# Kernel optimization log

Measured on AMD Instinct MI355X. Metric: run time of the kernel, lower is better.

## Reference

```python
import jax, jax.numpy as jnp
import numpy as np

F_IN = 512
F_OUT = 512
HEADS = 8  # all heads share the same weights in the original module
NEG_SLOPE = 0.01  # nn.LeakyReLU default
MASK_VAL = -1.0e10


def setup_inputs() -> dict:
    key = jax.random.key(0)
    ks = jax.random.split(key, 6)
    B, N = 8, 2048
    X_input = jax.random.normal(ks[0], (B, N, F_IN), dtype=jnp.float32)
    u = jax.random.uniform(ks[1], (B, N, N), dtype=jnp.float32)
    A_input = jnp.maximum((u < 0.02).astype(jnp.float32), jnp.eye(N, dtype=jnp.float32)[None])
    # learned params (nn.Linear stores W as [out,in]; we use [in,out] with x @ W)
    Wk = jax.random.normal(ks[2], (F_IN, F_OUT), dtype=jnp.float32) / np.sqrt(F_IN).astype(np.float32)
    bk = jnp.zeros((F_OUT,), dtype=jnp.float32)
    ws = jax.random.normal(ks[3], (F_OUT,), dtype=jnp.float32) / np.sqrt(F_OUT).astype(np.float32)
    bs = jnp.zeros((), dtype=jnp.float32)
    wn = jax.random.normal(ks[4], (F_OUT,), dtype=jnp.float32) / np.sqrt(F_OUT).astype(np.float32)
    bn = jnp.zeros((), dtype=jnp.float32)
    return {"X_input": X_input, "A_input": A_input, "Wk": Wk, "bk": bk,
            "ws": ws, "bs": bs, "wn": wn, "bn": bn}


def reference(X_input, A_input, Wk, bk, ws, bs, wn, bn):
    # shared projection (identical across all heads in the original loop)
    feat = jnp.einsum('bnf,fg->bng', X_input, Wk) + bk          # [B,N,F_]
    a_self = jnp.einsum('bng,g->bn', feat, ws) + bs             # [B,N]
    a_neigh = jnp.einsum('bng,g->bn', feat, wn) + bn            # [B,N]
    # torch.bmm([B,N,1],[B,1,N]) -> multiplicative outer product score
    att = jax.nn.leaky_relu(a_self[:, :, None] * a_neigh[:, None, :], NEG_SLOPE)
    att = att + MASK_VAL * (1.0 - A_input)                      # [B,N,N]
    p = jax.nn.softmax(att, axis=-1)
    nf = jnp.einsum('bij,bjg->big', p, feat)                    # [B,N,F_]
    # concat of HEADS identical head outputs, then tanh
    out = jnp.tanh(jnp.concatenate([nf] * HEADS, axis=-1))      # [B,N,HEADS*F_]
    return out
```

## Files before the change

### kernel.cpp

```cpp
#include <hip/hip_runtime.h>

#define NEG_SLOPE 0.01f
#define B_ 8
#define N_ 2048
#define F_ 512
#define M_ (B_ * N_)

typedef unsigned short u16;
typedef __attribute__((ext_vector_type(8))) unsigned short u16x8;
typedef __attribute__((ext_vector_type(8))) __bf16 bf16x8;
typedef __attribute__((ext_vector_type(4))) float f32x4;

__device__ __forceinline__ u16 f2bf(float f) {
    unsigned u = __float_as_uint(f);
    u += 0x7FFFu + ((u >> 16) & 1u);
    return (u16)(u >> 16);
}
__device__ __forceinline__ float bf2f(u16 h) {
    return __uint_as_float(((unsigned)h) << 16);
}

__device__ __forceinline__ f32x4 mfma16(u16x8 a, u16x8 b, f32x4 c) {
    return __builtin_amdgcn_mfma_f32_16x16x32_bf16(
        __builtin_bit_cast(bf16x8, a), __builtin_bit_cast(bf16x8, b), c, 0, 0, 0);
}

__device__ __forceinline__ void load_lds16(const void* g, void* l) {
    __builtin_amdgcn_global_load_lds(
        (__attribute__((address_space(1))) void*)(void*)g,
        (__attribute__((address_space(3))) void*)l, 16, 0, 0);
}

__global__ __launch_bounds__(256) void convert_wkt(const float* __restrict__ Wk,
                                                   u16* __restrict__ Whi,
                                                   u16* __restrict__ Wlo) {
    const int id = blockIdx.x * 256 + threadIdx.x;
    const int k = id & 511;
    const int n = id >> 9;
    const float f = Wk[k * 512 + n];
    const u16 h = f2bf(f);
    Whi[id] = h;
    Wlo[id] = f2bf(f - bf2f(h));
}

__global__ __launch_bounds__(256) void prep(const float* __restrict__ Wk,
                                            const float* __restrict__ bk,
                                            const float* __restrict__ ws,
                                            const float* __restrict__ bs,
                                            const float* __restrict__ wn,
                                            const float* __restrict__ bn,
                                            float* __restrict__ ws2,
                                            float* __restrict__ wn2,
                                            float* __restrict__ csn) {
    const int t = threadIdx.x, lane = t & 63, w = t >> 6;
    const int bid = blockIdx.x;
    if (bid >= 256) {
        if (w == 0) {
            const int sel = bid - 256;
            const float* vec = sel ? wn : ws;
            const float4 b0 = *(const float4*)(bk + lane * 8);
            const float4 b1 = *(const float4*)(bk + lane * 8 + 4);
            const float4 v0 = *(const float4*)(vec + lane * 8);
            const float4 v1 = *(const float4*)(vec + lane * 8 + 4);
            float d = b0.x * v0.x + b0.y * v0.y + b0.z * v0.z + b0.w * v0.w +
                      b1.x * v1.x + b1.y * v1.y + b1.z * v1.z + b1.w * v1.w;
#pragma unroll
            for (int m = 32; m; m >>= 1) d += __shfl_xor(d, m);
            if (lane == 0) csn[sel] = d + (sel ? bn[0] : bs[0]);
        }
        return;
    }
    const int W = bid * 4 + w;
    const int k = W & 511;
    const float* vec = (W < 512) ? ws : wn;
    const float4 w0 = *(const float4*)(Wk + (size_t)k * 512 + lane * 8);
    const float4 w1 = *(const float4*)(Wk + (size_t)k * 512 + lane * 8 + 4);
    const float4 v0 = *(const float4*)(vec + lane * 8);
    const float4 v1 = *(const float4*)(vec + lane * 8 + 4);
    float d = w0.x * v0.x + w0.y * v0.y + w0.z * v0.z + w0.w * v0.w +
              w1.x * v1.x + w1.y * v1.y + w1.z * v1.z + w1.w * v1.w;
#pragma unroll
    for (int m = 32; m; m >>= 1) d += __shfl_xor(d, m);
    if (lane == 0) ((W < 512) ? ws2 : wn2)[k] = d;
}

__global__ __launch_bounds__(256) void dots_x(const float* __restrict__ X,
                                              const float* __restrict__ ws2,
                                              const float* __restrict__ wn2,
                                              const float* __restrict__ csn,
                                              float* __restrict__ a_self,
                                              float* __restrict__ a_neigh) {
    const int t = threadIdx.x, lane = t & 63, w = t >> 6;
    const int row = blockIdx.x * 4 + w;
    const float4 f0 = *(const float4*)(X + (size_t)row * 512 + lane * 8);
    const float4 f1 = *(const float4*)(X + (size_t)row * 512 + lane * 8 + 4);
    const float fv[8] = {f0.x, f0.y, f0.z, f0.w, f1.x, f1.y, f1.z, f1.w};
    const float4 sa = *(const float4*)(ws2 + lane * 8);
    const float4 sb = *(const float4*)(ws2 + lane * 8 + 4);
    const float4 na = *(const float4*)(wn2 + lane * 8);
    const float4 nb = *(const float4*)(wn2 + lane * 8 + 4);
    float ds = fv[0] * sa.x + fv[1] * sa.y + fv[2] * sa.z + fv[3] * sa.w +
               fv[4] * sb.x + fv[5] * sb.y + fv[6] * sb.z + fv[7] * sb.w;
    float dn = fv[0] * na.x + fv[1] * na.y + fv[2] * na.z + fv[3] * na.w +
               fv[4] * nb.x + fv[5] * nb.y + fv[6] * nb.z + fv[7] * nb.w;
#pragma unroll
    for (int m = 32; m; m >>= 1) {
        ds += __shfl_xor(ds, m);
        dn += __shfl_xor(dn, m);
    }
    if (lane == 0) {
        a_self[row] = ds + csn[0];
        a_neigh[row] = dn + csn[1];
    }
}

__global__ __launch_bounds__(256) void gemm_feat(const float* __restrict__ X,
                                                 const u16* __restrict__ Whi,
                                                 const u16* __restrict__ Wlo,
                                                 const float* __restrict__ bk,
                                                 u16* __restrict__ feat) {
    __shared__ u16 Ah[128 * 64];
    __shared__ u16 Al[128 * 64];
    __shared__ u16 Bh[128 * 64];
    __shared__ u16 Bl[128 * 64];
    const int t = threadIdx.x;
    const int lane = t & 63;
    const int w = t >> 6;
    const int bid = blockIdx.x;
    const int tm = (bid & 7) * 16 + (bid >> 5);
    const int tn = (bid >> 3) & 3;
    const int wr = w >> 1, wc = w & 1;

    f32x4 acc[4][4];
#pragma unroll
    for (int m = 0; m < 4; ++m)
#pragma unroll
        for (int n = 0; n < 4; ++n) acc[m][n] = {0.f, 0.f, 0.f, 0.f};

    const int lrow = lane >> 3;
    const int lcol = (lane & 7) * 8;
    const u16* BhBase = Whi + ((size_t)(tn * 128 + w * 8 + lrow)) * 512 + lcol;
    const u16* BlBase = Wlo + ((size_t)(tn * 128 + w * 8 + lrow)) * 512 + lcol;
    u16* BhW = Bh + (w * 8) * 64;
    u16* BlW = Bl + (w * 8) * 64;

    const int arow = t >> 3;
    const int akk = (t & 7) * 8;
    const float* Abase = X + ((size_t)(tm * 128 + arow)) * 512 + akk;
    u16* AhW = Ah + arow * 64 + akk;
    u16* AlW = Al + arow * 64 + akk;

    for (int k0 = 0; k0 < 512; k0 += 64) {
#pragma unroll
        for (int iss = 0; iss < 4; ++iss) {
            load_lds16(BhBase + (size_t)(iss * 32) * 512 + k0, BhW + iss * 32 * 64);
            load_lds16(BlBase + (size_t)(iss * 32) * 512 + k0, BlW + iss * 32 * 64);
        }
#pragma unroll
        for (int p = 0; p < 4; ++p) {
            const float4 x0 = *(const float4*)(Abase + (size_t)(p * 32) * 512 + k0);
            const float4 x1 = *(const float4*)(Abase + (size_t)(p * 32) * 512 + k0 + 4);
            const float xv[8] = {x0.x, x0.y, x0.z, x0.w, x1.x, x1.y, x1.z, x1.w};
            u16x8 hi, lo;
#pragma unroll
            for (int e = 0; e < 8; ++e) {
                const u16 h = f2bf(xv[e]);
                hi[e] = h;
                lo[e] = f2bf(xv[e] - bf2f(h));
            }
            *(u16x8*)(AhW + p * 32 * 64) = hi;
            *(u16x8*)(AlW + p * 32 * 64) = lo;
        }
        __syncthreads();
#pragma unroll
        for (int kk = 0; kk < 64; kk += 32) {
            u16x8 ah[4], al[4], bh[4], bl[4];
            const int aoff = kk + (lane >> 4) * 8;
#pragma unroll
            for (int m = 0; m < 4; ++m) {
                const int r = (wr * 64 + m * 16 + (lane & 15)) * 64 + aoff;
                ah[m] = *(const u16x8*)(Ah + r);
                al[m] = *(const u16x8*)(Al + r);
            }
#pragma unroll
            for (int n = 0; n < 4; ++n) {
                const int r = (wc * 64 + n * 16 + (lane & 15)) * 64 + aoff;
                bh[n] = *(const u16x8*)(Bh + r);
                bl[n] = *(const u16x8*)(Bl + r);
            }
#pragma unroll
            for (int m = 0; m < 4; ++m)
#pragma unroll
                for (int n = 0; n < 4; ++n) {
                    acc[m][n] = mfma16(ah[m], bh[n], acc[m][n]);
                    acc[m][n] = mfma16(ah[m], bl[n], acc[m][n]);
                    acc[m][n] = mfma16(al[m], bh[n], acc[m][n]);
                }
        }
        __syncthreads();
    }

    const int crow0 = tm * 128 + wr * 64;
    const int ccol0 = tn * 128 + wc * 64;
#pragma unroll
    for (int n = 0; n < 4; ++n) {
        const int gc = ccol0 + n * 16 + (lane & 15);
        const float bkv = bk[gc];
#pragma unroll
        for (int m = 0; m < 4; ++m) {
            const int gr = crow0 + m * 16 + (lane >> 4) * 4;
#pragma unroll
            for (int r = 0; r < 4; ++r)
                feat[(size_t)(gr + r) * 512 + gc] = f2bf(acc[m][n][r] + bkv);
        }
    }
}

__global__ __launch_bounds__(256) void attn_row(const float* __restrict__ A,
                                                const u16* __restrict__ feat,
                                                const float* __restrict__ a_self,
                                                const float* __restrict__ a_neigh,
                                                float* __restrict__ out) {
    const int bid = blockIdx.x;
    const int row = (bid & 7) * N_ + (bid >> 3);
    const int b = bid & 7;
    const int t = threadIdx.x;
    const int lane = t & 63, w = t >> 6;

    __shared__ int   lj[N_];
    __shared__ float lsv[N_];
    __shared__ int   wtot[4];
    __shared__ float wred[8];
    __shared__ float nfw[4][F_];

    const float asi = a_self[row];

    const float4* Arow = (const float4*)(A + (size_t)row * N_);
    const float4* An   = (const float4*)(a_neigh + b * N_);
    const float4 a0 = Arow[t * 2], a1 = Arow[t * 2 + 1];
    const float4 n0 = An[t * 2],   n1 = An[t * 2 + 1];
    const float av[8] = {a0.x, a0.y, a0.z, a0.w, a1.x, a1.y, a1.z, a1.w};
    const float nv[8] = {n0.x, n0.y, n0.z, n0.w, n1.x, n1.y, n1.z, n1.w};
    float sv[8];
    int cnt = 0;
    float mloc = -3.0e38f;
#pragma unroll
    for (int e = 0; e < 8; ++e) {
        float s = asi * nv[e];
        s = s > 0.f ? s : NEG_SLOPE * s;
        sv[e] = s;
        if (av[e] != 0.f) { ++cnt; mloc = fmaxf(mloc, s); }
    }
    int v = cnt;
#pragma unroll
    for (int off = 1; off < 64; off <<= 1) {
        const int u = __shfl_up(v, off);
        if (lane >= off) v += u;
    }
#pragma unroll
    for (int m = 32; m; m >>= 1) mloc = fmaxf(mloc, __shfl_xor(mloc, m));
    if (lane == 63) wtot[w] = v;
    if (lane == 0) wred[w] = mloc;
    __syncthreads();
    int base = v - cnt;
#pragma unroll
    for (int i = 0; i < 4; ++i) base += (i < w) ? wtot[i] : 0;
    const int total = wtot[0] + wtot[1] + wtot[2] + wtot[3];
    const float mx = fmaxf(fmaxf(wred[0], wred[1]), fmaxf(wred[2], wred[3]));
    int pos = base;
#pragma unroll
    for (int e = 0; e < 8; ++e) {
        if (av[e] != 0.f) { lj[pos] = t * 8 + e; lsv[pos] = sv[e]; ++pos; }
    }
    __syncthreads();

    float ssum = 0.f;
    for (int k = t; k < total; k += 256) {
        const float wv = __expf(lsv[k] - mx);
        lsv[k] = wv;
        ssum += wv;
    }
#pragma unroll
    for (int m = 32; m; m >>= 1) ssum += __shfl_xor(ssum, m);
    if (lane == 0) wred[4 + w] = ssum;
    __syncthreads();
    const float inv = 1.f / (wred[4] + wred[5] + wred[6] + wred[7]);

    const u16* frow = feat + (size_t)b * N_ * F_ + lane * 8;
    float acc[8] = {0.f, 0.f, 0.f, 0.f, 0.f, 0.f, 0.f, 0.f};
    int k = w;
    for (; k + 4 < total; k += 8) {
        const size_t j0 = (size_t)lj[k] * F_, j1 = (size_t)lj[k + 4] * F_;
        const float p0 = lsv[k], p1 = lsv[k + 4];
        const u16x8 v0 = *(const u16x8*)(frow + j0);
        const u16x8 v1 = *(const u16x8*)(frow + j1);
#pragma unroll
        for (int e = 0; e < 8; ++e) acc[e] += p0 * bf2f(v0[e]) + p1 * bf2f(v1[e]);
    }
    if (k < total) {
        const size_t j0 = (size_t)lj[k] * F_;
        const float p0 = lsv[k];
        const u16x8 v0 = *(const u16x8*)(frow + j0);
#pragma unroll
        for (int e = 0; e < 8; ++e) acc[e] += p0 * bf2f(v0[e]);
    }
#pragma unroll
    for (int e = 0; e < 8; ++e) nfw[w][lane * 8 + e] = acc[e];
    __syncthreads();

    const int f0 = t * 2;
    const float nf0 = (nfw[0][f0] + nfw[1][f0]) + (nfw[2][f0] + nfw[3][f0]);
    const float nf1 = (nfw[0][f0 + 1] + nfw[1][f0 + 1]) + (nfw[2][f0 + 1] + nfw[3][f0 + 1]);
    const float o0 = tanhf(nf0 * inv);
    const float o1 = tanhf(nf1 * inv);
    const float2 o = make_float2(o0, o1);
    float* obase = out + (size_t)row * (8 * F_) + f0;
#pragma unroll
    for (int h = 0; h < 8; ++h) *(float2*)(obase + h * F_) = o;
}

extern "C" void kernel_launch(void* const* d_in, const int* in_sizes, int n_in,
                              void* d_out, int out_size, void* d_ws, size_t ws_size,
                              hipStream_t stream) {
    const float* X  = (const float*)d_in[0];
    const float* A  = (const float*)d_in[1];
    const float* Wk = (const float*)d_in[2];
    const float* bk = (const float*)d_in[3];
    const float* ws = (const float*)d_in[4];
    const float* bs = (const float*)d_in[5];
    const float* wn = (const float*)d_in[6];
    const float* bn = (const float*)d_in[7];
    float* out = (float*)d_out;

    char* wsb = (char*)d_ws;
    u16*   feat    = (u16*)(wsb);
    u16*   Whi     = (u16*)(wsb + 16777216);
    u16*   Wlo     = (u16*)(wsb + 17301504);
    float* a_self  = (float*)(wsb + 17825792);
    float* a_neigh = (float*)(wsb + 17891328);
    float* ws2     = (float*)(wsb + 17956864);
    float* wn2     = (float*)(wsb + 17958912);
    float* csn     = (float*)(wsb + 17960960);

    convert_wkt<<<dim3(1024),  dim3(256), 0, stream>>>(Wk, Whi, Wlo);
    prep       <<<dim3(258),   dim3(256), 0, stream>>>(Wk, bk, ws, bs, wn, bn, ws2, wn2, csn);
    dots_x     <<<dim3(4096),  dim3(256), 0, stream>>>(X, ws2, wn2, csn, a_self, a_neigh);
    gemm_feat  <<<dim3(512),   dim3(256), 0, stream>>>(X, Whi, Wlo, bk, feat);
    attn_row   <<<dim3(16384), dim3(256), 0, stream>>>(A, feat, a_self, a_neigh, out);
}
```

Before: 161.9 us.

## Switch feature GEMM to single-pass fp16 MFMA with swizzled LDS, fuse prep kernels

Replaces the three-pass bf16 hi/lo split GEMM with a single fp16 MFMA pass, which cuts both the MFMA count and the LDS traffic. It swizzles the LDS layout to avoid bank conflicts and merges the weight conversion and prep kernels into a single launch. Feat is now stored as fp16. The attention kernel now computes the exponentials during compaction and stores neighbor indices as u16, which removes a barrier and a pass over LDS. The GEMM loses precision compared with the split-bf16 scheme, and fp16 carries a risk of range overflow.

```diff
diff --git a/kernel.cpp b/kernel.cpp
--- a/kernel.cpp
+++ b/kernel.cpp
@@ -4,25 +4,15 @@
 #define B_ 8
 #define N_ 2048
 #define F_ 512
-#define M_ (B_ * N_)
 
 typedef unsigned short u16;
 typedef __attribute__((ext_vector_type(8))) unsigned short u16x8;
-typedef __attribute__((ext_vector_type(8))) __bf16 bf16x8;
+typedef __attribute__((ext_vector_type(8))) _Float16 f16x8;
 typedef __attribute__((ext_vector_type(4))) float f32x4;
 
-__device__ __forceinline__ u16 f2bf(float f) {
-    unsigned u = __float_as_uint(f);
-    u += 0x7FFFu + ((u >> 16) & 1u);
-    return (u16)(u >> 16);
-}
-__device__ __forceinline__ float bf2f(u16 h) {
-    return __uint_as_float(((unsigned)h) << 16);
-}
-
-__device__ __forceinline__ f32x4 mfma16(u16x8 a, u16x8 b, f32x4 c) {
-    return __builtin_amdgcn_mfma_f32_16x16x32_bf16(
-        __builtin_bit_cast(bf16x8, a), __builtin_bit_cast(bf16x8, b), c, 0, 0, 0);
+__device__ __forceinline__ f32x4 mfma16f(u16x8 a, u16x8 b, f32x4 c) {
+    return __builtin_amdgcn_mfma_f32_16x16x32_f16(
+        __builtin_bit_cast(f16x8, a), __builtin_bit_cast(f16x8, b), c, 0, 0, 0);
 }
 
 __device__ __forceinline__ void load_lds16(const void* g, void* l) {
@@ -31,32 +21,27 @@
         (__attribute__((address_space(3))) void*)l, 16, 0, 0);
 }
 
-__global__ __launch_bounds__(256) void convert_wkt(const float* __restrict__ Wk,
-                                                   u16* __restrict__ Whi,
-                                                   u16* __restrict__ Wlo) {
-    const int id = blockIdx.x * 256 + threadIdx.x;
-    const int k = id & 511;
-    const int n = id >> 9;
-    const float f = Wk[k * 512 + n];
-    const u16 h = f2bf(f);
-    Whi[id] = h;
-    Wlo[id] = f2bf(f - bf2f(h));
-}
-
-__global__ __launch_bounds__(256) void prep(const float* __restrict__ Wk,
-                                            const float* __restrict__ bk,
-                                            const float* __restrict__ ws,
-                                            const float* __restrict__ bs,
-                                            const float* __restrict__ wn,
-                                            const float* __restrict__ bn,
-                                            float* __restrict__ ws2,
-                                            float* __restrict__ wn2,
-                                            float* __restrict__ csn) {
-    const int t = threadIdx.x, lane = t & 63, w = t >> 6;
-    const int bid = blockIdx.x;
-    if (bid >= 256) {
+__global__ __launch_bounds__(256) void prep_all(const float* __restrict__ Wk,
+                                                const float* __restrict__ bk,
+                                                const float* __restrict__ ws,
+                                                const float* __restrict__ bs,
+                                                const float* __restrict__ wn,
+                                                const float* __restrict__ bn,
+                                                u16* __restrict__ Wf,
+                                                float* __restrict__ ws2,
+                                                float* __restrict__ wn2,
+                                                float* __restrict__ csn) {
+    const int bid = blockIdx.x, t = threadIdx.x;
+    if (bid < 1024) {
+        const int id = bid * 256 + t;
+        const int k = id & 511, n = id >> 9;
+        ((_Float16*)Wf)[id] = (_Float16)Wk[k * 512 + n];
+        return;
+    }
+    const int lane = t & 63, w = t >> 6;
+    if (bid >= 1280) {
         if (w == 0) {
-            const int sel = bid - 256;
+            const int sel = bid - 1280;
             const float* vec = sel ? wn : ws;
             const float4 b0 = *(const float4*)(bk + lane * 8);
             const float4 b1 = *(const float4*)(bk + lane * 8 + 4);
@@ -70,7 +55,7 @@
         }
         return;
     }
-    const int W = bid * 4 + w;
+    const int W = (bid - 1024) * 4 + w;
     const int k = W & 511;
     const float* vec = (W < 512) ? ws : wn;
     const float4 w0 = *(const float4*)(Wk + (size_t)k * 512 + lane * 8);
@@ -82,6 +67,89 @@
 #pragma unroll
     for (int m = 32; m; m >>= 1) d += __shfl_xor(d, m);
     if (lane == 0) ((W < 512) ? ws2 : wn2)[k] = d;
+}
+
+__global__ __launch_bounds__(256) void gemm_feat(const float* __restrict__ X,
+                                                 const u16* __restrict__ Wf,
+                                                 const float* __restrict__ bk,
+                                                 u16* __restrict__ feat) {
+    __shared__ u16 Af[128 * 64];
+    __shared__ u16 Bf[128 * 64];
+    const int t = threadIdx.x;
+    const int lane = t & 63;
+    const int w = t >> 6;
+    const int bid = blockIdx.x;
+    const int tm = (bid & 7) * 16 + (bid >> 5);
+    const int tn = (bid >> 3) & 3;
+    const int wr = w >> 1, wc = w & 1;
+
+    f32x4 acc[4][4];
+#pragma unroll
+    for (int m = 0; m < 4; ++m)
+#pragma unroll
+        for (int n = 0; n < 4; ++n) acc[m][n] = {0.f, 0.f, 0.f, 0.f};
+
+    const int lrow = lane >> 3;
+    const int scol = ((lane & 7) ^ lrow) * 8;
+    const u16* Bbase = Wf + ((size_t)(tn * 128 + w * 8 + lrow)) * 512 + scol;
+    u16* BfW = Bf + (w * 8) * 64;
+
+    const int arow = t >> 3;
+    const int akk = (t & 7) * 8;
+    const float* Abase = X + ((size_t)(tm * 128 + arow)) * 512 + akk;
+    u16* AfW = Af + arow * 64 + (akk ^ ((arow & 7) * 8));
+
+    for (int k0 = 0; k0 < 512; k0 += 64) {
+#pragma unroll
+        for (int iss = 0; iss < 4; ++iss)
+            load_lds16(Bbase + (size_t)(iss * 32) * 512 + k0, BfW + iss * 32 * 64);
+#pragma unroll
+        for (int p = 0; p < 4; ++p) {
+            const float4 x0 = *(const float4*)(Abase + (size_t)(p * 32) * 512 + k0);
+            const float4 x1 = *(const float4*)(Abase + (size_t)(p * 32) * 512 + k0 + 4);
+            const float xv[8] = {x0.x, x0.y, x0.z, x0.w, x1.x, x1.y, x1.z, x1.w};
+            u16x8 hv;
+#pragma unroll
+            for (int e = 0; e < 8; ++e)
+                hv[e] = __builtin_bit_cast(u16, (_Float16)xv[e]);
+            *(u16x8*)(AfW + p * 32 * 64) = hv;
+        }
+        __syncthreads();
+        const int swz = (lane & 7) * 8;
+#pragma unroll
+        for (int kk = 0; kk < 64; kk += 32) {
+            u16x8 af[4], bf[4];
+            const int aoff = (kk + (lane >> 4) * 8) ^ swz;
+#pragma unroll
+            for (int m = 0; m < 4; ++m)
+                af[m] = *(const u16x8*)(Af + (wr * 64 + m * 16 + (lane & 15)) * 64 + aoff);
+#pragma unroll
+            for (int n = 0; n < 4; ++n)
+                bf[n] = *(const u16x8*)(Bf + (wc * 64 + n * 16 + (lane & 15)) * 64 + aoff);
+#pragma unroll
+            for (int m = 0; m < 4; ++m)
+#pragma unroll
+                for (int n = 0; n < 4; ++n)
+                    acc[m][n] = mfma16f(af[m], bf[n], acc[m][n]);
+        }
+        __syncthreads();
+    }
+
+    const int crow0 = tm * 128 + wr * 64;
+    const int ccol0 = tn * 128 + wc * 64;
+    _Float16* feat16 = (_Float16*)feat;
+#pragma unroll
+    for (int n = 0; n < 4; ++n) {
+        const int gc = ccol0 + n * 16 + (lane & 15);
+        const float bkv = bk[gc];
+#pragma unroll
+        for (int m = 0; m < 4; ++m) {
+            const int gr = crow0 + m * 16 + (lane >> 4) * 4;
+#pragma unroll
+            for (int r = 0; r < 4; ++r)
+                feat16[(size_t)(gr + r) * 512 + gc] = (_Float16)(acc[m][n][r] + bkv);
+        }
+    }
 }
 
 __global__ __launch_bounds__(256) void dots_x(const float* __restrict__ X,
@@ -114,108 +182,6 @@
     }
 }
 
-__global__ __launch_bounds__(256) void gemm_feat(const float* __restrict__ X,
-                                                 const u16* __restrict__ Whi,
-                                                 const u16* __restrict__ Wlo,
-                                                 const float* __restrict__ bk,
-                                                 u16* __restrict__ feat) {
-    __shared__ u16 Ah[128 * 64];
-    __shared__ u16 Al[128 * 64];
-    __shared__ u16 Bh[128 * 64];
-    __shared__ u16 Bl[128 * 64];
-    const int t = threadIdx.x;
-    const int lane = t & 63;
-    const int w = t >> 6;
-    const int bid = blockIdx.x;
-    const int tm = (bid & 7) * 16 + (bid >> 5);
-    const int tn = (bid >> 3) & 3;
-    const int wr = w >> 1, wc = w & 1;
-
-    f32x4 acc[4][4];
-#pragma unroll
-    for (int m = 0; m < 4; ++m)
-#pragma unroll
-        for (int n = 0; n < 4; ++n) acc[m][n] = {0.f, 0.f, 0.f, 0.f};
-
-    const int lrow = lane >> 3;
-    const int lcol = (lane & 7) * 8;
-    const u16* BhBase = Whi + ((size_t)(tn * 128 + w * 8 + lrow)) * 512 + lcol;
-    const u16* BlBase = Wlo + ((size_t)(tn * 128 + w * 8 + lrow)) * 512 + lcol;
-    u16* BhW = Bh + (w * 8) * 64;
-    u16* BlW = Bl + (w * 8) * 64;
-
-    const int arow = t >> 3;
-    const int akk = (t & 7) * 8;
-    const float* Abase = X + ((size_t)(tm * 128 + arow)) * 512 + akk;
-    u16* AhW = Ah + arow * 64 + akk;
-    u16* AlW = Al + arow * 64 + akk;
-
-    for (int k0 = 0; k0 < 512; k0 += 64) {
-#pragma unroll
-        for (int iss = 0; iss < 4; ++iss) {
-            load_lds16(BhBase + (size_t)(iss * 32) * 512 + k0, BhW + iss * 32 * 64);
-            load_lds16(BlBase + (size_t)(iss * 32) * 512 + k0, BlW + iss * 32 * 64);
-        }
-#pragma unroll
-        for (int p = 0; p < 4; ++p) {
-            const float4 x0 = *(const float4*)(Abase + (size_t)(p * 32) * 512 + k0);
-            const float4 x1 = *(const float4*)(Abase + (size_t)(p * 32) * 512 + k0 + 4);
-            const float xv[8] = {x0.x, x0.y, x0.z, x0.w, x1.x, x1.y, x1.z, x1.w};
-            u16x8 hi, lo;
-#pragma unroll
-            for (int e = 0; e < 8; ++e) {
-                const u16 h = f2bf(xv[e]);
-                hi[e] = h;
-                lo[e] = f2bf(xv[e] - bf2f(h));
-            }
-            *(u16x8*)(AhW + p * 32 * 64) = hi;
-            *(u16x8*)(AlW + p * 32 * 64) = lo;
-        }
-        __syncthreads();
-#pragma unroll
-        for (int kk = 0; kk < 64; kk += 32) {
-            u16x8 ah[4], al[4], bh[4], bl[4];
-            const int aoff = kk + (lane >> 4) * 8;
-#pragma unroll
-            for (int m = 0; m < 4; ++m) {
-                const int r = (wr * 64 + m * 16 + (lane & 15)) * 64 + aoff;
-                ah[m] = *(const u16x8*)(Ah + r);
-                al[m] = *(const u16x8*)(Al + r);
-            }
-#pragma unroll
-            for (int n = 0; n < 4; ++n) {
-                const int r = (wc * 64 + n * 16 + (lane & 15)) * 64 + aoff;
-                bh[n] = *(const u16x8*)(Bh + r);
-                bl[n] = *(const u16x8*)(Bl + r);
-            }
-#pragma unroll
-            for (int m = 0; m < 4; ++m)
-#pragma unroll
-                for (int n = 0; n < 4; ++n) {
-                    acc[m][n] = mfma16(ah[m], bh[n], acc[m][n]);
-                    acc[m][n] = mfma16(ah[m], bl[n], acc[m][n]);
-                    acc[m][n] = mfma16(al[m], bh[n], acc[m][n]);
-                }
-        }
-        __syncthreads();
-    }
-
-    const int crow0 = tm * 128 + wr * 64;
-    const int ccol0 = tn * 128 + wc * 64;
-#pragma unroll
-    for (int n = 0; n < 4; ++n) {
-        const int gc = ccol0 + n * 16 + (lane & 15);
-        const float bkv = bk[gc];
-#pragma unroll
-        for (int m = 0; m < 4; ++m) {
-            const int gr = crow0 + m * 16 + (lane >> 4) * 4;
-#pragma unroll
-            for (int r = 0; r < 4; ++r)
-                feat[(size_t)(gr + r) * 512 + gc] = f2bf(acc[m][n][r] + bkv);
-        }
-    }
-}
-
 __global__ __launch_bounds__(256) void attn_row(const float* __restrict__ A,
                                                 const u16* __restrict__ feat,
                                                 const float* __restrict__ a_self,
@@ -227,7 +193,7 @@
     const int t = threadIdx.x;
     const int lane = t & 63, w = t >> 6;
 
-    __shared__ int   lj[N_];
+    __shared__ u16   lj[N_];
     __shared__ float lsv[N_];
     __shared__ int   wtot[4];
     __shared__ float wred[8];
@@ -267,18 +233,18 @@
     for (int i = 0; i < 4; ++i) base += (i < w) ? wtot[i] : 0;
     const int total = wtot[0] + wtot[1] + wtot[2] + wtot[3];
     const float mx = fmaxf(fmaxf(wred[0], wred[1]), fmaxf(wred[2], wred[3]));
+
+    float ssum = 0.f;
     int pos = base;
 #pragma unroll
     for (int e = 0; e < 8; ++e) {
-        if (av[e] != 0.f) { lj[pos] = t * 8 + e; lsv[pos] = sv[e]; ++pos; }
-    }
-    __syncthreads();
-
-    float ssum = 0.f;
-    for (int k = t; k < total; k += 256) {
-        const float wv = __expf(lsv[k] - mx);
-        lsv[k] = wv;
-        ssum += wv;
+        if (av[e] != 0.f) {
+            const float wv = __expf(sv[e] - mx);
+            lj[pos] = (u16)(t * 8 + e);
+            lsv[pos] = wv;
+            ssum += wv;
+            ++pos;
+        }
     }
 #pragma unroll
     for (int m = 32; m; m >>= 1) ssum += __shfl_xor(ssum, m);
@@ -292,17 +258,17 @@
     for (; k + 4 < total; k += 8) {
         const size_t j0 = (size_t)lj[k] * F_, j1 = (size_t)lj[k + 4] * F_;
         const float p0 = lsv[k], p1 = lsv[k + 4];
-        const u16x8 v0 = *(const u16x8*)(frow + j0);
-        const u16x8 v1 = *(const u16x8*)(frow + j1);
-#pragma unroll
-        for (int e = 0; e < 8; ++e) acc[e] += p0 * bf2f(v0[e]) + p1 * bf2f(v1[e]);
+        const f16x8 v0 = *(const f16x8*)(frow + j0);
+        const f16x8 v1 = *(const f16x8*)(frow + j1);
+#pragma unroll
+        for (int e = 0; e < 8; ++e) acc[e] += p0 * (float)v0[e] + p1 * (float)v1[e];
     }
     if (k < total) {
         const size_t j0 = (size_t)lj[k] * F_;
         const float p0 = lsv[k];
-        const u16x8 v0 = *(const u16x8*)(frow + j0);
-#pragma unroll
-        for (int e = 0; e < 8; ++e) acc[e] += p0 * bf2f(v0[e]);
+        const f16x8 v0 = *(const f16x8*)(frow + j0);
+#pragma unroll
+        for (int e = 0; e < 8; ++e) acc[e] += p0 * (float)v0[e];
     }
 #pragma unroll
     for (int e = 0; e < 8; ++e) nfw[w][lane * 8 + e] = acc[e];
@@ -334,17 +300,15 @@
 
     char* wsb = (char*)d_ws;
     u16*   feat    = (u16*)(wsb);
-    u16*   Whi     = (u16*)(wsb + 16777216);
-    u16*   Wlo     = (u16*)(wsb + 17301504);
-    float* a_self  = (float*)(wsb + 17825792);
-    float* a_neigh = (float*)(wsb + 17891328);
-    float* ws2     = (float*)(wsb + 17956864);
-    float* wn2     = (float*)(wsb + 17958912);
-    float* csn     = (float*)(wsb + 17960960);
-
-    convert_wkt<<<dim3(1024),  dim3(256), 0, stream>>>(Wk, Whi, Wlo);
-    prep       <<<dim3(258),   dim3(256), 0, stream>>>(Wk, bk, ws, bs, wn, bn, ws2, wn2, csn);
+    u16*   Wf      = (u16*)(wsb + 16777216);
+    float* a_self  = (float*)(wsb + 17301504);
+    float* a_neigh = (float*)(wsb + 17367040);
+    float* ws2     = (float*)(wsb + 17432576);
+    float* wn2     = (float*)(wsb + 17434624);
+    float* csn     = (float*)(wsb + 17436672);
+
+    prep_all   <<<dim3(1282),  dim3(256), 0, stream>>>(Wk, bk, ws, bs, wn, bn, Wf, ws2, wn2, csn);
+    gemm_feat  <<<dim3(512),   dim3(256), 0, stream>>>(X, Wf, bk, feat);
     dots_x     <<<dim3(4096),  dim3(256), 0, stream>>>(X, ws2, wn2, csn, a_self, a_neigh);
-    gemm_feat  <<<dim3(512),   dim3(256), 0, stream>>>(X, Whi, Wlo, bk, feat);
     attn_row   <<<dim3(16384), dim3(256), 0, stream>>>(A, feat, a_self, a_neigh, out);
 }
```

Measured after the change: 146.2 us. 1.11x faster.
